# Performance work log

Hardware: AMD Instinct MI355X
Metric: run time of the kernel (lower is better)

The kernel has to match this reference:

```python
import jax, jax.numpy as jnp
import numpy as np

M = 4          # num_models
B = 128        # per-model batch
C = 10         # num_classes
K = 32         # num_centroids
F = 512        # feature_dimension
NZ = 512       # noise_dimension
H = 512        # hidden_dimension
SIGMA = 1.0    # length_scale (not learnable)


def be_fc(x, W, r, s, b=None):
    # BatchEnsemble (Ensemble_orderFC): x is [M*N, in], rows ordered by model.
    N = x.shape[0] // M
    xm = x.reshape(M, N, -1) * r[:, None, :]
    out = jnp.einsum('mni,io->mno', xm, W) * s[:, None, :]
    if b is not None:
        out = out + b[:, None, :]
    return out.reshape(M * N, -1)


def setup_inputs() -> dict:
    key = jax.random.key(0)
    ks = jax.random.split(key, 16)
    sc = lambda fan_in: 1.0 / np.sqrt(fan_in)
    inp = {
        'x': jax.random.normal(ks[0], (M * B, F), dtype=jnp.float32),
        'proto_noise': jax.random.normal(ks[1], (C * K, NZ), dtype=jnp.float32),
        # layer_W: F -> F*C, bias=False
        'W_lw': jax.random.normal(ks[2], (F, F * C), dtype=jnp.float32) * sc(F),
        'r_lw': 1.0 + 0.1 * jax.random.normal(ks[3], (M, F), dtype=jnp.float32),
        's_lw': 1.0 + 0.1 * jax.random.normal(ks[4], (M, F * C), dtype=jnp.float32),
        # fc1_p: (C + NZ) -> H
        'W1': jax.random.normal(ks[5], (C + NZ, H), dtype=jnp.float32) * sc(C + NZ),
        'r1': 1.0 + 0.1 * jax.random.normal(ks[6], (M, C + NZ), dtype=jnp.float32),
        's1': 1.0 + 0.1 * jax.random.normal(ks[7], (M, H), dtype=jnp.float32),
        'b1': jnp.zeros((M, H), dtype=jnp.float32),
        # fc2_p: H -> F
        'W2': jax.random.normal(ks[8], (H, F), dtype=jnp.float32) * sc(H),
        'r2': 1.0 + 0.1 * jax.random.normal(ks[9], (M, H), dtype=jnp.float32),
        's2': 1.0 + 0.1 * jax.random.normal(ks[10], (M, F), dtype=jnp.float32),
        'b2': jnp.zeros((M, F), dtype=jnp.float32),
    }
    return inp


def reference(x, proto_noise, W_lw, r_lw, s_lw, W1, r1, s1, b1, W2, r2, s2, b2):
    # ---- get_prototype ----
    onehot = jnp.repeat(jnp.eye(C, dtype=x.dtype), K, axis=0)        # [C*K, C]
    proto_in = jnp.concatenate([proto_noise, onehot], axis=1)        # [C*K, NZ+C]
    proto_in = jnp.tile(proto_in, (M, 1))                            # [M*C*K, NZ+C]
    h = jax.nn.relu(be_fc(proto_in, W1, r1, s1, b1))
    proto = be_fc(h, W2, r2, s2, b2).reshape(M, C, K, F)

    # ---- last_layer ----
    z = be_fc(x, W_lw, r_lw, s_lw)                                   # [M*B, F*C]
    z = z.reshape(M * B, F, C)

    # ---- output_layer: broadcast RBF squared-distance reduction ----
    zt = jnp.transpose(z.reshape(M, B, F, C), (0, 1, 3, 2))          # [M, B, C, F]
    diff = zt[:, :, :, None, :] - proto[:, None, :, :, :]            # [M, B, C, K, F]
    distances = -(diff ** 2).mean(axis=(-1, -2)) / (2.0 * SIGMA ** 2)  # [M, B, C]

    logit = distances.reshape(-1, C)                                 # [M*B, C]
    return jnp.exp(logit)
```

## Files before the change

### kernel.cpp

```cpp
#include <hip/hip_runtime.h>
#include <math.h>

#define MM 4
#define BB 128
#define CC 10
#define KK 32
#define FF 512
#define HH 512
#define NP 320
#define OUTW 5120

using bf16x8 = __attribute__((ext_vector_type(8))) short;
using f32x4  = __attribute__((ext_vector_type(4))) float;

__device__ __forceinline__ unsigned short f2bf(float f) {
    unsigned int u = __float_as_uint(f);
    u += 0x7FFFu + ((u >> 16) & 1u);
    return (unsigned short)(u >> 16);
}

template<int EPI, int ASRC, int BSRC, int WR, int WC, int I, int J,
         int KSTEPS, int KREALB, int RPM, int NCOLS>
__device__ __forceinline__ void gemm_tile(
    const int bx, const int by,
    const unsigned short* __restrict__ Abf, const float* __restrict__ Af32,
    const float* __restrict__ ascale,
    const unsigned short* __restrict__ Btbf, const float* __restrict__ Bf32,
    const float* __restrict__ s, const float* __restrict__ bias,
    const float* __restrict__ auxr, void* __restrict__ outv,
    float* __restrict__ auxw, unsigned short* smem)
{
    constexpr int TR = WR * I * 16;
    constexpr int TC = WC * J * 16;
    static_assert(TR <= 64 && TC == 64, "staging geometry");
    constexpr int BUFE = (TR + TC) * 32;
    const int t = threadIdx.x;
    const int lane = t & 63;
    const int w = t >> 6;
    const int wr = w / WC, wc = w % WC;
    const int l15 = lane & 15, l4 = lane >> 4;
    const int rowT = by * TR, colT = bx * TC;
    const int m = rowT / RPM;

    constexpr bool AGUARD = (TR * 4 < 256);
    const bool aact = !AGUARD || (t < TR * 4);
    const int asrow = t >> 2, ag = t & 3;
    const int stA = asrow * 32 + ((ag ^ ((asrow >> 1) & 3)) * 8);
    const unsigned short* gA = nullptr;
    const float* gAf = nullptr;
    const float* scp = nullptr;
    int cn = 0;
    if constexpr (ASRC == 0) {
        if (aact) gA = Abf + (size_t)(rowT + asrow) * 512 + ag * 8;
    } else {
        static_assert(TR == 64, "ASRC2 needs TR==64");
        gAf = Af32 + (size_t)((rowT % NP) + asrow) * 512 + ag * 8;
        scp = ascale + (size_t)m * 522 + ag * 8;
        cn = ((rowT % NP) + asrow) >> 5;
    }
    const int bsrow = t >> 2, bg = t & 3;
    const int stB0 = bsrow * 32 + ((bg ^ ((bsrow >> 1) & 3)) * 8);
    const int bcol = t & 63, bkg = t >> 6;
    const int stB1 = bcol * 32 + ((bkg ^ ((bcol >> 1) & 3)) * 8);
    const unsigned short* gB = nullptr;
    if constexpr (BSRC == 0)
        gB = Btbf + (size_t)(colT + bsrow) * 512 + bg * 8;

    int offA[I], offB[J];
#pragma unroll
    for (int i = 0; i < I; ++i) {
        const int rA = wr * (I * 16) + i * 16 + l15;
        offA[i] = rA * 32 + ((l4 ^ ((rA >> 1) & 3)) * 8);
    }
#pragma unroll
    for (int j = 0; j < J; ++j) {
        const int rB = wc * (J * 16) + j * 16 + l15;
        offB[j] = rB * 32 + ((l4 ^ ((rB >> 1) & 3)) * 8);
    }

    f32x4 acc[I][J];
#pragma unroll
    for (int i = 0; i < I; ++i)
#pragma unroll
        for (int j = 0; j < J; ++j) acc[i][j] = (f32x4){0.f, 0.f, 0.f, 0.f};

    uint4 ra, rb;
    float4 nf0, nf1, ns0, ns1;
    float rbf[8];

#define FETCH(KS)                                                              \
    {                                                                          \
        const int k0_ = (KS) * 32;                                             \
        if constexpr (ASRC == 0) {                                             \
            if (aact) ra = *(const uint4*)(gA + k0_);                          \
        } else {                                                               \
            if (k0_ < 512) {                                                   \
                nf0 = *(const float4*)(gAf + k0_);                             \
                nf1 = *(const float4*)(gAf + k0_ + 4);                         \
                ns0 = *(const float4*)(scp + k0_);                             \
                ns1 = *(const float4*)(scp + k0_ + 4);                         \
            }                                                                  \
        }                                                                      \
        if constexpr (BSRC == 0) {                                             \
            rb = *(const uint4*)(gB + k0_);                                    \
        } else {                                                               \
            _Pragma("unroll")                                                  \
            for (int q = 0; q < 8; ++q) {                                      \
                const int gk = k0_ + bkg * 8 + q;                              \
                rbf[q] = (gk < KREALB)                                         \
                    ? Bf32[(size_t)gk * NCOLS + colT + bcol] : 0.f;            \
            }                                                                  \
        }                                                                      \
    }

#define WRITE(KS, BUF)                                                         \
    {                                                                          \
        const int k0_ = (KS) * 32;                                             \
        unsigned short* As_ = smem + (BUF) * BUFE;                             \
        unsigned short* Bs_ = As_ + TR * 32;                                   \
        if constexpr (ASRC == 0) {                                             \
            if (aact) *(uint4*)(As_ + stA) = ra;                               \
        } else {                                                               \
            union { unsigned short us[8]; uint4 q4; } o;                       \
            if (k0_ < 512) {                                                   \
                float vv[8] = {nf0.x, nf0.y, nf0.z, nf0.w,                     \
                               nf1.x, nf1.y, nf1.z, nf1.w};                    \
                float ss[8] = {ns0.x, ns0.y, ns0.z, ns0.w,                     \
                               ns1.x, ns1.y, ns1.z, ns1.w};                    \
                _Pragma("unroll")                                              \
                for (int q = 0; q < 8; ++q) o.us[q] = f2bf(vv[q] * ss[q]);     \
            } else {                                                           \
                _Pragma("unroll")                                              \
                for (int q = 0; q < 8; ++q) {                                  \
                    const int gk = k0_ + ag * 8 + q;                           \
                    float v = (gk < 522 && (gk - 512) == cn)                   \
                        ? ascale[(size_t)m * 522 + gk] : 0.f;                  \
                    o.us[q] = f2bf(v);                                         \
                }                                                              \
            }                                                                  \
            *(uint4*)(As_ + stA) = o.q4;                                       \
        }                                                                      \
        if constexpr (BSRC == 0) {                                             \
            *(uint4*)(Bs_ + stB0) = rb;                                        \
        } else {                                                               \
            union { unsigned short us[8]; uint4 q4; } ob;                      \
            _Pragma("unroll")                                                  \
            for (int q = 0; q < 8; ++q) ob.us[q] = f2bf(rbf[q]);               \
            *(uint4*)(Bs_ + stB1) = ob.q4;                                     \
        }                                                                      \
    }

    FETCH(0);
    WRITE(0, 0);
    __syncthreads();

#pragma unroll 1
    for (int ks = 0; ks < KSTEPS; ++ks) {
        const int cur = ks & 1;
        if (ks + 1 < KSTEPS) FETCH(ks + 1);
        const unsigned short* As_ = smem + cur * BUFE;
        const unsigned short* Bs_ = As_ + TR * 32;
        bf16x8 af[I], bfv[J];
#pragma unroll
        for (int i = 0; i < I; ++i) af[i] = *(const bf16x8*)(As_ + offA[i]);
#pragma unroll
        for (int j = 0; j < J; ++j) bfv[j] = *(const bf16x8*)(Bs_ + offB[j]);
#pragma unroll
        for (int i = 0; i < I; ++i)
#pragma unroll
            for (int j = 0; j < J; ++j)
                acc[i][j] = __builtin_amdgcn_mfma_f32_16x16x32_bf16(
                    af[i], bfv[j], acc[i][j], 0, 0, 0);
        if (ks + 1 < KSTEPS) {
            WRITE(ks + 1, cur ^ 1);
            __syncthreads();
        }
    }
#undef FETCH
#undef WRITE

    if constexpr (EPI == 0) {
#pragma unroll
        for (int j = 0; j < J; ++j) {
            const int col = colT + wc * (J * 16) + j * 16 + l15;
            const float sv = s[(size_t)m * NCOLS + col];
            const float bv = bias[(size_t)m * NCOLS + col];
            const float rv = auxr[(size_t)m * NCOLS + col];
#pragma unroll
            for (int i = 0; i < I; ++i)
#pragma unroll
                for (int ir = 0; ir < 4; ++ir) {
                    const int row = rowT + wr * (I * 16) + i * 16 + l4 * 4 + ir;
                    float v = fmaxf(acc[i][j][ir] * sv + bv, 0.f) * rv;
                    ((unsigned short*)outv)[(size_t)row * NCOLS + col] = f2bf(v);
                }
        }
    } else if constexpr (EPI == 1) {
        static_assert(WR == 1 && I == 2 && J == 1, "EPI1 geometry");
        const int mq = rowT / NP;
        const int c = (rowT % NP) / KK;
        const int mc = mq * CC + c;
        const int col = colT + wc * 16 + l15;
        const float sv = s[(size_t)mq * NCOLS + col];
        const float bv = bias[(size_t)mq * NCOLS + col];
        float cs = 0.f, sq = 0.f;
#pragma unroll
        for (int i = 0; i < I; ++i)
#pragma unroll
            for (int ir = 0; ir < 4; ++ir) {
                float v = acc[i][0][ir] * sv + bv;
                cs += v;
                sq += v * v;
            }
        cs += __shfl_xor(cs, 16, 64);
        cs += __shfl_xor(cs, 32, 64);
        if (l4 == 0) ((float*)outv)[(size_t)mc * FF + col] = cs;
#pragma unroll
        for (int off = 1; off < 64; off <<= 1) sq += __shfl_xor(sq, off, 64);
        if (lane == 0) auxw[mc * 32 + bx * 4 + w] = sq;
    } else {
        static_assert(WR == 2 && WC == 2 && I == 2 && J == 2, "EPI2 geometry");
        const int cb = colT >> 9;
        const int slot = ((bx & 7) << 1) | wc;
        float sv[J], pv[J];
#pragma unroll
        for (int j = 0; j < J; ++j) {
            const int col = colT + wc * (J * 16) + j * 16 + l15;
            sv[j] = s[(size_t)m * NCOLS + (col & 511) * 10 + (col >> 9)];
            pv[j] = bias[(size_t)m * NCOLS + col];
        }
        float* dst = (float*)outv;
#pragma unroll
        for (int i = 0; i < I; ++i)
#pragma unroll
            for (int ir = 0; ir < 4; ++ir) {
                const int row = rowT + wr * (I * 16) + i * 16 + l4 * 4 + ir;
                float znv = 0.f, crv = 0.f;
#pragma unroll
                for (int j = 0; j < J; ++j) {
                    float v = acc[i][j][ir] * sv[j];
                    znv += v * v;
                    crv += v * pv[j];
                }
#pragma unroll
                for (int off = 1; off < 16; off <<= 1) {
                    znv += __shfl_xor(znv, off, 64);
                    crv += __shfl_xor(crv, off, 64);
                }
                if (l15 == 0) {
                    float2 o = {znv, crv};
                    *(float2*)(dst + ((size_t)(row * CC + cb) * 16 + slot) * 2) = o;
                }
            }
    }
}

__global__ __launch_bounds__(256) void k_phase1(
    const float* __restrict__ noise, const float* __restrict__ r1,
    const float* __restrict__ W1, const float* __restrict__ s1,
    const float* __restrict__ b1, const float* __restrict__ r2,
    unsigned short* __restrict__ A2)
{
    __shared__ __align__(16) unsigned short smem[8192];
    gemm_tile<0, 2, 1, 2, 2, 2, 2, 17, 522, NP, HH>(
        blockIdx.x % 8, blockIdx.x / 8, nullptr, noise, r1, nullptr, W1,
        s1, b1, r2, (void*)A2, nullptr, smem);
}

__global__ __launch_bounds__(256) void k_phase2(
    const unsigned short* __restrict__ A2, const float* __restrict__ W2,
    const float* __restrict__ s2, const float* __restrict__ b2,
    const float* __restrict__ W_lw, const float* __restrict__ x,
    const float* __restrict__ r_lw,
    float* __restrict__ psum, float* __restrict__ pn_part,
    unsigned short* __restrict__ Wlwt, unsigned short* __restrict__ xr)
{
    __shared__ __align__(16) unsigned short smem[6144];
    const int blk = blockIdx.x;
    const int t = threadIdx.x;
    if (blk < 320) {
        gemm_tile<1, 0, 1, 1, 4, 2, 1, 16, 512, NP, FF>(
            blk % 8, blk / 8, A2, nullptr, nullptr, nullptr, W2,
            s2, b2, nullptr, (void*)psum, pn_part, smem);
    } else if (blk < 960) {
        unsigned short (*T)[65] = (unsigned short (*)[65])smem;
        const int bb = blk - 320;
        const int n0 = (bb % 80) * 64, k0 = (bb / 80) * 64;
#pragma unroll
        for (int p = 0; p < 4; ++p) {
            int kk = (t >> 4) + p * 16;
            int nn = (t & 15) * 4;
            float4 v = *(const float4*)(W_lw + (size_t)(k0 + kk) * OUTW + n0 + nn);
            T[nn + 0][kk] = f2bf(v.x);
            T[nn + 1][kk] = f2bf(v.y);
            T[nn + 2][kk] = f2bf(v.z);
            T[nn + 3][kk] = f2bf(v.w);
        }
        __syncthreads();
#pragma unroll
        for (int p = 0; p < 2; ++p) {
            int n = (t >> 3) + p * 32;
            int kg = t & 7;
            union { unsigned short us[8]; uint4 v; } o;
#pragma unroll
            for (int q = 0; q < 8; ++q) o.us[q] = T[n][kg * 8 + q];
            int gn = n0 + n;
            int dr = (gn % 10) * 512 + gn / 10;
            *(uint4*)(Wlwt + (size_t)dr * 512 + k0 + kg * 8) = o.v;
        }
    } else {
        const int id = (blk - 960) * 256 + t;
        const int row = id >> 6, g = id & 63;
        const int mq = row >> 7;
        const float* xp = x + (size_t)row * 512 + g * 8;
        const float* rp = r_lw + (size_t)mq * 512 + g * 8;
        union { unsigned short us[8]; uint4 v; } o;
#pragma unroll
        for (int q = 0; q < 8; ++q) o.us[q] = f2bf(xp[q] * rp[q]);
        *(uint4*)(xr + (size_t)row * 512 + g * 8) = o.v;
    }
}

__global__ __launch_bounds__(256) void k_phase3(
    const unsigned short* __restrict__ xr, const unsigned short* __restrict__ Wlwt,
    const float* __restrict__ s_lw, const float* __restrict__ psum,
    float* __restrict__ dist_part)
{
    __shared__ __align__(16) unsigned short smem[8192];
    gemm_tile<2, 0, 0, 2, 2, 2, 2, 16, 512, BB, OUTW>(
        blockIdx.x, blockIdx.y, xr, nullptr, nullptr, Wlwt, nullptr,
        s_lw, psum, nullptr, (void*)dist_part, nullptr, smem);
}

__global__ __launch_bounds__(256) void k_out(
    const float* __restrict__ dist_part, const float* __restrict__ pn_part,
    float* __restrict__ out)
{
    const int id = blockIdx.x * 256 + threadIdx.x;
    const int c = id % 10;
    const int mb = id / 10;
    const int mc = (mb >> 7) * 10 + c;
    const float* dp = dist_part + (size_t)id * 32;
    float zn = 0.f, cr = 0.f;
#pragma unroll
    for (int q = 0; q < 16; ++q) {
        zn += dp[q * 2];
        cr += dp[q * 2 + 1];
    }
    float pnv = 0.f;
#pragma unroll
    for (int q = 0; q < 32; ++q) pnv += pn_part[mc * 32 + q];
    const float inv = 1.f / (2.f * (float)KK * (float)FF);
    out[id] = expf(-((float)KK * zn - 2.f * cr + pnv) * inv);
}

extern "C" void kernel_launch(void* const* d_in, const int* in_sizes, int n_in,
                              void* d_out, int out_size, void* d_ws, size_t ws_size,
                              hipStream_t stream) {
    const float* x     = (const float*)d_in[0];
    const float* noise = (const float*)d_in[1];
    const float* W_lw  = (const float*)d_in[2];
    const float* r_lw  = (const float*)d_in[3];
    const float* s_lw  = (const float*)d_in[4];
    const float* W1    = (const float*)d_in[5];
    const float* r1    = (const float*)d_in[6];
    const float* s1    = (const float*)d_in[7];
    const float* b1    = (const float*)d_in[8];
    const float* W2    = (const float*)d_in[9];
    const float* r2    = (const float*)d_in[10];
    const float* s2    = (const float*)d_in[11];
    const float* b2    = (const float*)d_in[12];
    float* out = (float*)d_out;

    char* base = (char*)d_ws;
    float* psum          = (float*)(base + 0);
    float* pn_part       = (float*)(base + 81920);
    float* dist_part     = (float*)(base + 87040);
    unsigned short* A2   = (unsigned short*)(base + 742400);
    unsigned short* xr   = (unsigned short*)(base + 2053120);
    unsigned short* Wlwt = (unsigned short*)(base + 2577408);

    k_phase1<<<160, 256, 0, stream>>>(noise, r1, W1, s1, b1, r2, A2);
    k_phase2<<<1088, 256, 0, stream>>>(A2, W2, s2, b2, W_lw, x, r_lw,
                                       psum, pn_part, Wlwt, xr);
    k_phase3<<<dim3(80, 8), 256, 0, stream>>>(xr, Wlwt, s_lw, psum, dist_part);
    k_out<<<20, 256, 0, stream>>>(dist_part, pn_part, out);
}
```

Measured before the change: 54.63 us.

## Fold output reduction into phase3 via atomic ticket, move x scaling to phase1

```diff
diff --git a/kernel.cpp b/kernel.cpp
--- a/kernel.cpp
+++ b/kernel.cpp
@@ -259,21 +259,37 @@
     const float* __restrict__ noise, const float* __restrict__ r1,
     const float* __restrict__ W1, const float* __restrict__ s1,
     const float* __restrict__ b1, const float* __restrict__ r2,
-    unsigned short* __restrict__ A2)
+    const float* __restrict__ x, const float* __restrict__ r_lw,
+    unsigned short* __restrict__ A2, unsigned short* __restrict__ xr,
+    unsigned int* __restrict__ ticket)
 {
     __shared__ __align__(16) unsigned short smem[8192];
-    gemm_tile<0, 2, 1, 2, 2, 2, 2, 17, 522, NP, HH>(
-        blockIdx.x % 8, blockIdx.x / 8, nullptr, noise, r1, nullptr, W1,
-        s1, b1, r2, (void*)A2, nullptr, smem);
+    const int b = blockIdx.x;
+    const int t = threadIdx.x;
+    if (b < 160) {
+        gemm_tile<0, 2, 1, 2, 2, 2, 2, 17, 522, NP, HH>(
+            b % 8, b / 8, nullptr, noise, r1, nullptr, W1,
+            s1, b1, r2, (void*)A2, nullptr, smem);
+    } else {
+        const int id = (b - 160) * 256 + t;
+        const int row = id >> 6, g = id & 63;
+        const int mq = row >> 7;
+        const float* xp = x + (size_t)row * 512 + g * 8;
+        const float* rp = r_lw + (size_t)mq * 512 + g * 8;
+        union { unsigned short us[8]; uint4 v; } o;
+#pragma unroll
+        for (int q = 0; q < 8; ++q) o.us[q] = f2bf(xp[q] * rp[q]);
+        *(uint4*)(xr + (size_t)row * 512 + g * 8) = o.v;
+        if (b == 160 && t == 0) *ticket = 0u;
+    }
 }
 
 __global__ __launch_bounds__(256) void k_phase2(
     const unsigned short* __restrict__ A2, const float* __restrict__ W2,
     const float* __restrict__ s2, const float* __restrict__ b2,
-    const float* __restrict__ W_lw, const float* __restrict__ x,
-    const float* __restrict__ r_lw,
+    const float* __restrict__ W_lw,
     float* __restrict__ psum, float* __restrict__ pn_part,
-    unsigned short* __restrict__ Wlwt, unsigned short* __restrict__ xr)
+    unsigned short* __restrict__ Wlwt)
 {
     __shared__ __align__(16) unsigned short smem[6144];
     const int blk = blockIdx.x;
@@ -282,7 +298,7 @@
         gemm_tile<1, 0, 1, 1, 4, 2, 1, 16, 512, NP, FF>(
             blk % 8, blk / 8, A2, nullptr, nullptr, nullptr, W2,
             s2, b2, nullptr, (void*)psum, pn_part, smem);
-    } else if (blk < 960) {
+    } else {
         unsigned short (*T)[65] = (unsigned short (*)[65])smem;
         const int bb = blk - 320;
         const int n0 = (bb % 80) * 64, k0 = (bb / 80) * 64;
@@ -308,50 +324,54 @@
             int dr = (gn % 10) * 512 + gn / 10;
             *(uint4*)(Wlwt + (size_t)dr * 512 + k0 + kg * 8) = o.v;
         }
-    } else {
-        const int id = (blk - 960) * 256 + t;
-        const int row = id >> 6, g = id & 63;
-        const int mq = row >> 7;
-        const float* xp = x + (size_t)row * 512 + g * 8;
-        const float* rp = r_lw + (size_t)mq * 512 + g * 8;
-        union { unsigned short us[8]; uint4 v; } o;
-#pragma unroll
-        for (int q = 0; q < 8; ++q) o.us[q] = f2bf(xp[q] * rp[q]);
-        *(uint4*)(xr + (size_t)row * 512 + g * 8) = o.v;
     }
 }
 
 __global__ __launch_bounds__(256) void k_phase3(
     const unsigned short* __restrict__ xr, const unsigned short* __restrict__ Wlwt,
     const float* __restrict__ s_lw, const float* __restrict__ psum,
-    float* __restrict__ dist_part)
+    float* __restrict__ dist_part, const float* __restrict__ pn_part,
+    unsigned int* __restrict__ ticket, float* __restrict__ out)
 {
     __shared__ __align__(16) unsigned short smem[8192];
-    gemm_tile<2, 0, 0, 2, 2, 2, 2, 16, 512, BB, OUTW>(
-        blockIdx.x, blockIdx.y, xr, nullptr, nullptr, Wlwt, nullptr,
-        s_lw, psum, nullptr, (void*)dist_part, nullptr, smem);
-}
-
-__global__ __launch_bounds__(256) void k_out(
-    const float* __restrict__ dist_part, const float* __restrict__ pn_part,
-    float* __restrict__ out)
-{
-    const int id = blockIdx.x * 256 + threadIdx.x;
-    const int c = id % 10;
-    const int mb = id / 10;
-    const int mc = (mb >> 7) * 10 + c;
-    const float* dp = dist_part + (size_t)id * 32;
-    float zn = 0.f, cr = 0.f;
-#pragma unroll
-    for (int q = 0; q < 16; ++q) {
-        zn += dp[q * 2];
-        cr += dp[q * 2 + 1];
-    }
-    float pnv = 0.f;
-#pragma unroll
-    for (int q = 0; q < 32; ++q) pnv += pn_part[mc * 32 + q];
-    const float inv = 1.f / (2.f * (float)KK * (float)FF);
-    out[id] = expf(-((float)KK * zn - 2.f * cr + pnv) * inv);
+    const int blk = blockIdx.x;
+    const int t = threadIdx.x;
+    if (blk < 640) {
+        gemm_tile<2, 0, 0, 2, 2, 2, 2, 16, 512, BB, OUTW>(
+            blk % 80, blk / 80, xr, nullptr, nullptr, Wlwt, nullptr,
+            s_lw, psum, nullptr, (void*)dist_part, nullptr, smem);
+        __syncthreads();
+        if (t == 0) {
+            __threadfence();
+            __hip_atomic_fetch_add(ticket, 1u, __ATOMIC_RELEASE,
+                                   __HIP_MEMORY_SCOPE_AGENT);
+        }
+    } else {
+        if (t == 0) {
+            while (__hip_atomic_load(ticket, __ATOMIC_ACQUIRE,
+                                     __HIP_MEMORY_SCOPE_AGENT) < 640u)
+                __builtin_amdgcn_s_sleep(8);
+        }
+        __syncthreads();
+        __threadfence();
+        const int id = (blk - 640) * 256 + t;
+        const int c = id % 10;
+        const int mc = ((id / 10) >> 7) * 10 + c;
+        const float* dp = dist_part + (size_t)id * 32;
+        float zn = 0.f, cr = 0.f;
+#pragma unroll
+        for (int q = 0; q < 16; ++q) {
+            zn += __hip_atomic_load((float*)&dp[q * 2], __ATOMIC_RELAXED,
+                                    __HIP_MEMORY_SCOPE_AGENT);
+            cr += __hip_atomic_load((float*)&dp[q * 2 + 1], __ATOMIC_RELAXED,
+                                    __HIP_MEMORY_SCOPE_AGENT);
+        }
+        float pnv = 0.f;
+#pragma unroll
+        for (int q = 0; q < 32; ++q) pnv += pn_part[mc * 32 + q];
+        const float inv = 1.f / (2.f * (float)KK * (float)FF);
+        out[id] = expf(-((float)KK * zn - 2.f * cr + pnv) * inv);
+    }
 }
 
 extern "C" void kernel_launch(void* const* d_in, const int* in_sizes, int n_in,
@@ -376,13 +396,15 @@
     float* psum          = (float*)(base + 0);
     float* pn_part       = (float*)(base + 81920);
     float* dist_part     = (float*)(base + 87040);
-    unsigned short* A2   = (unsigned short*)(base + 742400);
-    unsigned short* xr   = (unsigned short*)(base + 2053120);
-    unsigned short* Wlwt = (unsigned short*)(base + 2577408);
-
-    k_phase1<<<160, 256, 0, stream>>>(noise, r1, W1, s1, b1, r2, A2);
-    k_phase2<<<1088, 256, 0, stream>>>(A2, W2, s2, b2, W_lw, x, r_lw,
-                                       psum, pn_part, Wlwt, xr);
-    k_phase3<<<dim3(80, 8), 256, 0, stream>>>(xr, Wlwt, s_lw, psum, dist_part);
-    k_out<<<20, 256, 0, stream>>>(dist_part, pn_part, out);
-}
+    unsigned int* ticket = (unsigned int*)(base + 742400);
+    unsigned short* A2   = (unsigned short*)(base + 742656);
+    unsigned short* xr   = (unsigned short*)(base + 2053376);
+    unsigned short* Wlwt = (unsigned short*)(base + 2577664);
+
+    k_phase1<<<288, 256, 0, stream>>>(noise, r1, W1, s1, b1, r2, x, r_lw,
+                                      A2, xr, ticket);
+    k_phase2<<<960, 256, 0, stream>>>(A2, W2, s2, b2, W_lw,
+                                      psum, pn_part, Wlwt);
+    k_phase3<<<660, 256, 0, stream>>>(xr, Wlwt, s_lw, psum, dist_part,
+                                      pn_part, ticket, out);
+}
```

Result: slower. 89.07 us (+63.0%).
